# Optimization experiments

Measured on AMD Instinct MI355X. Metric: run time of the kernel, lower is better.

Reference implementation:

```python
import jax, jax.numpy as jnp
import numpy as np

B, T, C, H = 4, 2048, 1024, 16


def setup_inputs() -> dict:
    key = jax.random.key(0)
    k0, k1, k2 = jax.random.split(key, 3)
    s = C ** -0.5
    return {
        "x": jax.random.normal(k0, (B, T, C), jnp.float32),
        "Wqkv": jax.random.normal(k1, (C, 3 * C), jnp.float32) * s,
        "bqkv": jnp.zeros((3 * C,), jnp.float32),
        "Wo": jax.random.normal(k2, (C, C), jnp.float32) * s,
        "bo": jnp.zeros((C,), jnp.float32),
        "decoder": 1,
    }


def reference(x, Wqkv, bqkv, Wo, bo, decoder):
    Bx, Tx, Cx = x.shape
    d = Cx // H  # head dim
    qkv = x @ Wqkv + bqkv  # [B,T,3C]
    q, k, v = jnp.split(qkv, 3, axis=-1)
    q = q.reshape(Bx, Tx, H, d).transpose(0, 2, 1, 3)  # [B,H,T,d]
    k = k.reshape(Bx, Tx, H, d).transpose(0, 2, 1, 3)
    v = v.reshape(Bx, Tx, H, d).transpose(0, 2, 1, 3)
    # Source: qk / embd_dim**(-0.5)  ==  qk * sqrt(embd_dim)  (faithful quirk)
    scale = jnp.asarray(Cx ** 0.5, x.dtype)
    qk = jnp.einsum("bhqd,bhkd->bhqk", q, k) * scale  # [B,H,T,T]
    if decoder:  # decoder is a Python int constant
        tril = jnp.tril(jnp.ones((Tx, Tx), bool))
        qk = jnp.where(tril, qk, -jnp.inf)
    attn = jax.nn.softmax(qk, axis=-1)
    out = jnp.einsum("bhqk,bhkd->bhqd", attn, v)  # [B,H,T,d]
    out = out.transpose(0, 2, 1, 3).reshape(Bx, Tx, Cx)
    return out @ Wo + bo
```

## Files before the change

### kernel.cpp

```cpp
#include <hip/hip_runtime.h>
#include <cstdint>
#include <cstddef>

#define T_SEQ 2048
#define CEMB  1024
#define NHEAD 16
#define DHEAD 64

#define QSCALE 46.1662413084468f

typedef __attribute__((ext_vector_type(8))) short bf16x8;
typedef __attribute__((ext_vector_type(4))) float f32x4;

static __device__ __forceinline__ unsigned short f2bf(float x) {
    unsigned u = __builtin_bit_cast(unsigned, x);
    unsigned r = (u + 0x7FFFu + ((u >> 16) & 1u)) >> 16;
    return (unsigned short)r;
}
static __device__ __forceinline__ float bf2f(unsigned short b) {
    unsigned u = ((unsigned)b) << 16;
    return __builtin_bit_cast(float, u);
}

static __device__ __forceinline__ void gload16(const short* gsrc, short* ldsbase) {
    __builtin_amdgcn_global_load_lds(
        (const __attribute__((address_space(1))) void*)gsrc,
        (__attribute__((address_space(3))) void*)ldsbase, 16, 0, 0);
}

template<int SPLIT, bool A_F32, int OUT_MODE>
__global__ __launch_bounds__(256) void gemm_mfma_kernel(
    const float* __restrict__ Af, const short* __restrict__ Ah,
    const short* __restrict__ Bh, const short* __restrict__ Bl,
    const float* __restrict__ bias,
    void* __restrict__ Cout, void* __restrict__ Cout2, int K, int ldc)
{
    __shared__ __align__(16) short smem[(SPLIT == 3) ? 16384 : 8192];

    const int tid = threadIdx.x;
    const int w = tid >> 6, l = tid & 63;
    const int lr = l & 15, lg = l >> 4;
    const int wr = w >> 1, wc = w & 1;
    const int row0 = blockIdx.y * 128;
    const int col0 = blockIdx.x * 128;

    f32x4 acc[4][4];
    #pragma unroll
    for (int mt = 0; mt < 4; ++mt)
        #pragma unroll
        for (int nt = 0; nt < 4; ++nt)
            acc[mt][nt] = (f32x4){0.f, 0.f, 0.f, 0.f};

    const int sB0 = w * 128 + l, sB1 = sB0 + 64;
    const short* gB0 = Bh + (size_t)(col0 + (sB0 & 127)) * K + (sB0 >> 7) * 8;
    const short* gB1 = Bh + (size_t)(col0 + (sB1 & 127)) * K + (sB1 >> 7) * 8;
    short* dB0 = &smem[4096 + (w * 128) * 8];
    short* dB1 = &smem[4096 + (w * 128 + 64) * 8];
    const short* gBl0 = nullptr; const short* gBl1 = nullptr;
    if constexpr (SPLIT == 3) {
        gBl0 = Bl + (size_t)(col0 + (sB0 & 127)) * K + (sB0 >> 7) * 8;
        gBl1 = Bl + (size_t)(col0 + (sB1 & 127)) * K + (sB1 >> 7) * 8;
    }
    const short* gA0 = nullptr; const short* gA1 = nullptr;
    if constexpr (!A_F32) {
        gA0 = Ah + (size_t)(row0 + (sB0 & 127)) * K + (sB0 >> 7) * 8;
        gA1 = Ah + (size_t)(row0 + (sB1 & 127)) * K + (sB1 >> 7) * 8;
    }
    short* dA0 = &smem[(w * 128) * 8];
    short* dA1 = &smem[(w * 128 + 64) * 8];

    const int arow = tid >> 1, ahalf = tid & 1;
    const float* gAf = A_F32 ? (Af + (size_t)(row0 + arow) * K + ahalf * 16) : nullptr;

    for (int kt = 0; kt < K; kt += 32) {
        __syncthreads();
        if constexpr (!A_F32) {
            gload16(gA0 + kt, dA0);
            gload16(gA1 + kt, dA1);
        }
        gload16(gB0 + kt, dB0);
        gload16(gB1 + kt, dB1);
        if constexpr (SPLIT == 3) {
            gload16(gBl0 + kt, &smem[12288 + (w * 128) * 8]);
            gload16(gBl1 + kt, &smem[12288 + (w * 128 + 64) * 8]);
        }
        if constexpr (A_F32) {
            const float* src = gAf + kt;
            float4 f0 = *(const float4*)(src);
            float4 f1 = *(const float4*)(src + 4);
            float4 f2 = *(const float4*)(src + 8);
            float4 f3 = *(const float4*)(src + 12);
            float xs[16] = {f0.x, f0.y, f0.z, f0.w, f1.x, f1.y, f1.z, f1.w,
                            f2.x, f2.y, f2.z, f2.w, f3.x, f3.y, f3.z, f3.w};
            #pragma unroll
            for (int q = 0; q < 2; ++q) {
                bf16x8 h8, l8;
                #pragma unroll
                for (int e = 0; e < 8; ++e) {
                    float x = xs[q * 8 + e];
                    if constexpr (SPLIT == 3) {
                        unsigned u = __builtin_bit_cast(unsigned, x);
                        h8[e] = (short)(unsigned short)(u >> 16);
                        float hf = __builtin_bit_cast(float, u & 0xFFFF0000u);
                        l8[e] = (short)f2bf(x - hf);
                    } else {
                        h8[e] = (short)f2bf(x);
                    }
                }
                int slot = (ahalf * 2 + q) * 128 + arow;
                *(bf16x8*)&smem[slot * 8] = h8;
                if constexpr (SPLIT == 3) *(bf16x8*)&smem[8192 + slot * 8] = l8;
            }
        }
        __syncthreads();

        const int aoff = (lg * 128 + wr * 64 + lr) * 8;
        const int boff = 4096 + (lg * 128 + wc * 64 + lr) * 8;
        bf16x8 ahf[4], alf[4];
        #pragma unroll
        for (int mt = 0; mt < 4; ++mt) {
            ahf[mt] = *(const bf16x8*)&smem[aoff + mt * 128];
            if constexpr (SPLIT == 3)
                alf[mt] = *(const bf16x8*)&smem[8192 + aoff + mt * 128];
        }
        #pragma unroll
        for (int nt = 0; nt < 4; ++nt) {
            bf16x8 bhf = *(const bf16x8*)&smem[boff + nt * 128];
            if constexpr (SPLIT == 3) {
                bf16x8 blf = *(const bf16x8*)&smem[8192 + boff + nt * 128];
                #pragma unroll
                for (int mt = 0; mt < 4; ++mt) {
                    acc[mt][nt] = __builtin_amdgcn_mfma_f32_16x16x32_bf16(ahf[mt], bhf, acc[mt][nt], 0, 0, 0);
                    acc[mt][nt] = __builtin_amdgcn_mfma_f32_16x16x32_bf16(alf[mt], bhf, acc[mt][nt], 0, 0, 0);
                    acc[mt][nt] = __builtin_amdgcn_mfma_f32_16x16x32_bf16(ahf[mt], blf, acc[mt][nt], 0, 0, 0);
                }
            } else {
                #pragma unroll
                for (int mt = 0; mt < 4; ++mt)
                    acc[mt][nt] = __builtin_amdgcn_mfma_f32_16x16x32_bf16(ahf[mt], bhf, acc[mt][nt], 0, 0, 0);
            }
        }
    }

    #pragma unroll
    for (int mt = 0; mt < 4; ++mt) {
        #pragma unroll
        for (int r = 0; r < 4; ++r) {
            int m = row0 + wr * 64 + mt * 16 + lg * 4 + r;
            #pragma unroll
            for (int nt = 0; nt < 4; ++nt) {
                int n = col0 + wc * 64 + nt * 16 + lr;
                float v = acc[mt][nt][r] + bias[n];
                if constexpr (OUT_MODE == 0) {
                    ((float*)Cout)[(size_t)m * ldc + n] = v;
                } else if constexpr (OUT_MODE == 1) {
                    ((short*)Cout)[(size_t)m * ldc + n] = (short)f2bf(v);
                } else {
                    if (n < 1024) v *= QSCALE;
                    unsigned u = __builtin_bit_cast(unsigned, v);
                    ((short*)Cout)[(size_t)m * ldc + n] = (short)(unsigned short)(u >> 16);
                    float hf = __builtin_bit_cast(float, u & 0xFFFF0000u);
                    ((short*)Cout2)[(size_t)m * ldc + n] = (short)f2bf(v - hf);
                }
            }
        }
    }
}

__global__ __launch_bounds__(256) void transpose_split_kernel(
    const float* __restrict__ src, int nsrc,
    short* __restrict__ hi, short* __restrict__ lo)
{
    __shared__ float tile[64][68];
    const int tid = threadIdx.x;
    const int n0 = blockIdx.x * 64, k0 = blockIdx.y * 64;
    {
        int kr = tid >> 2, cg = tid & 3;
        const float* s = src + (size_t)(k0 + kr) * nsrc + n0 + cg * 16;
        #pragma unroll
        for (int q = 0; q < 4; ++q) {
            float4 f = *(const float4*)(s + q * 4);
            tile[kr][cg * 16 + q * 4 + 0] = f.x;
            tile[kr][cg * 16 + q * 4 + 1] = f.y;
            tile[kr][cg * 16 + q * 4 + 2] = f.z;
            tile[kr][cg * 16 + q * 4 + 3] = f.w;
        }
    }
    __syncthreads();
    {
        int nr = tid >> 2, kg = tid & 3;
        int n = n0 + nr;
        bf16x8 h0, h1, lo0, lo1;
        #pragma unroll
        for (int e = 0; e < 8; ++e) {
            float a = tile[kg * 16 + e][nr];
            float b = tile[kg * 16 + 8 + e][nr];
            unsigned short ha = f2bf(a), hb = f2bf(b);
            h0[e] = (short)ha; h1[e] = (short)hb;
            lo0[e] = (short)f2bf(a - bf2f(ha));
            lo1[e] = (short)f2bf(b - bf2f(hb));
        }
        short* dh = hi + (size_t)n * 1024 + k0 + kg * 16;
        *(bf16x8*)dh = h0;
        *(bf16x8*)(dh + 8) = h1;
        if (lo) {
            short* dl = lo + (size_t)n * 1024 + k0 + kg * 16;
            *(bf16x8*)dl = lo0;
            *(bf16x8*)(dl + 8) = lo1;
        }
    }
}

__global__ __launch_bounds__(256) void repack_vt_kernel(
    const short* __restrict__ v, short* __restrict__ vt)
{
    __shared__ short tile[64][80];
    const int tid = threadIdx.x;
    const int tt = blockIdx.x, h = blockIdx.y, b = blockIdx.z;
    const int t0 = tt * 64;
    {
        int tr = tid >> 2, cgrp = tid & 3;
        const short* src = v + (size_t)(b * T_SEQ + t0 + tr) * CEMB + h * DHEAD + cgrp * 16;
        *(bf16x8*)&tile[tr][cgrp * 16]     = *(const bf16x8*)src;
        *(bf16x8*)&tile[tr][cgrp * 16 + 8] = *(const bf16x8*)(src + 8);
    }
    __syncthreads();
    {
        int d = tid >> 2, tc = tid & 3;
        short s[16];
        #pragma unroll
        for (int e = 0; e < 16; ++e) s[e] = tile[tc * 16 + e][d];
        short* dst = vt + ((size_t)((b * NHEAD + h) * DHEAD + d)) * T_SEQ + t0 + tc * 16;
        bf16x8 v0, v1;
        #pragma unroll
        for (int e = 0; e < 8; ++e) { v0[e] = s[e]; v1[e] = s[8 + e]; }
        *(bf16x8*)dst       = v0;
        *(bf16x8*)(dst + 8) = v1;
    }
}

__global__ __launch_bounds__(256) void attn_mfma_kernel(
    const short* __restrict__ qkhi, const short* __restrict__ qklo,
    const short* __restrict__ vt, short* __restrict__ ctxb)
{
    __shared__ __align__(16) short smem[16384];

    const int tid = threadIdx.x;
    const int w = tid >> 6, l = tid & 63;
    const int lr = l & 15, lg = l >> 4;

    const int bid = blockIdx.x;
    const int p  = bid >> 6;
    const int bh = bid & 63;
    const int h = bh & 15, b = bh >> 4;
    const size_t bT = (size_t)b * T_SEQ;

    const int g0 = w * 128 + l, g1 = g0 + 64;
    const int rg0 = g0 >> 3, rg1 = g1 >> 3;
    const int sc0 = (g0 & 7) ^ (rg0 & 7), sc1 = (g1 & 7) ^ (rg1 & 7);
    short* const dst0 = &smem[(w * 128) * 8];
    short* const dst1 = &smem[(w * 128 + 64) * 8];

    const size_t koff0 = (bT + rg0) * 2048 + 1024 + h * DHEAD + sc0 * 8;
    const size_t koff1 = (bT + rg1) * 2048 + 1024 + h * DHEAD + sc1 * 8;
    const short* const pKh0 = qkhi + koff0;
    const short* const pKh1 = qkhi + koff1;
    const short* const pKl0 = qklo + koff0;
    const short* const pKl1 = qklo + koff1;
    const short* const pV0 = vt + ((size_t)((b * NHEAD + h) * DHEAD) + rg0) * T_SEQ + sc0 * 8;
    const short* const pV1 = vt + ((size_t)((b * NHEAD + h) * DHEAD) + rg1) * T_SEQ + sc1 * 8;

    const int psBase = 12288 + w * 1024;
    const int pwChunk = (lg >> 1);
    const int pwIntra = (lg & 1) * 4;

    for (int half = 0; half < 2; ++half) {
        const int xi = half ? (31 - p) : p;
        const int q0 = xi * 64;
        const int qw = q0 + w * 16;

        bf16x8 qhi[2], qlo[2];
        #pragma unroll
        for (int kk = 0; kk < 2; ++kk) {
            size_t off = (bT + qw + lr) * 2048 + h * DHEAD + kk * 32 + lg * 8;
            qhi[kk] = *(const bf16x8*)(qkhi + off);
            qlo[kk] = *(const bf16x8*)(qklo + off);
        }

        f32x4 O[4];
        #pragma unroll
        for (int dt = 0; dt < 4; ++dt)
            O[dt] = (f32x4){0.f, 0.f, 0.f, 0.f};
        float mrow = -3.0e38f;
        float lrow = 0.f;

        const int nsteps = xi + 1;
        for (int t = 0; t < nsteps; ++t) {
            const int j0 = t * 64;
            __syncthreads();
            gload16(pKh0 + (size_t)j0 * 2048, dst0);
            gload16(pKh1 + (size_t)j0 * 2048, dst1);
            gload16(pKl0 + (size_t)j0 * 2048, dst0 + 4096);
            gload16(pKl1 + (size_t)j0 * 2048, dst1 + 4096);
            gload16(pV0 + j0, dst0 + 8192);
            gload16(pV1 + j0, dst1 + 8192);
            __syncthreads();

            f32x4 St[4];
            #pragma unroll
            for (int ct = 0; ct < 4; ++ct) {
                f32x4 s = (f32x4){0.f, 0.f, 0.f, 0.f};
                #pragma unroll
                for (int kk = 0; kk < 2; ++kk) {
                    int j  = ct * 16 + lr;
                    int ck = kk * 4 + lg;
                    int idx = j * 64 + ((ck ^ (j & 7)) << 3);
                    bf16x8 kh8 = *(bf16x8*)&smem[idx];
                    bf16x8 kl8 = *(bf16x8*)&smem[4096 + idx];
                    s = __builtin_amdgcn_mfma_f32_16x16x32_bf16(kh8, qhi[kk], s, 0, 0, 0);
                    s = __builtin_amdgcn_mfma_f32_16x16x32_bf16(kh8, qlo[kk], s, 0, 0, 0);
                    s = __builtin_amdgcn_mfma_f32_16x16x32_bf16(kl8, qhi[kk], s, 0, 0, 0);
                }
                if (j0 + ct * 16 + 15 > qw) {
                    #pragma unroll
                    for (int r = 0; r < 4; ++r) {
                        int jabs = j0 + ct * 16 + lg * 4 + r;
                        int qabs = qw + lr;
                        s[r] = (jabs <= qabs) ? s[r] : -3.0e38f;
                    }
                }
                St[ct] = s;
            }

            float tm = fmaxf(fmaxf(fmaxf(St[0][0], St[0][1]), fmaxf(St[0][2], St[0][3])),
                             fmaxf(fmaxf(St[1][0], St[1][1]), fmaxf(St[1][2], St[1][3])));
            tm = fmaxf(tm, fmaxf(fmaxf(fmaxf(St[2][0], St[2][1]), fmaxf(St[2][2], St[2][3])),
                                 fmaxf(fmaxf(St[3][0], St[3][1]), fmaxf(St[3][2], St[3][3]))));
            tm = fmaxf(tm, __shfl_xor(tm, 16));
            tm = fmaxf(tm, __shfl_xor(tm, 32));

            if (__any(tm > mrow)) {
                float mnew  = fmaxf(mrow, tm);
                float alpha = __builtin_amdgcn_exp2f(mrow - mnew);
                mrow = mnew;
                lrow *= alpha;
                #pragma unroll
                for (int r = 0; r < 4; ++r) {
                    float aO = __shfl(alpha, lg * 4 + r);
                    #pragma unroll
                    for (int dt = 0; dt < 4; ++dt)
                        O[dt][r] *= aO;
                }
            }

            #pragma unroll
            for (int ct = 0; ct < 4; ++ct) {
                float p0 = __builtin_amdgcn_exp2f(St[ct][0] - mrow);
                float p1 = __builtin_amdgcn_exp2f(St[ct][1] - mrow);
                float p2 = __builtin_amdgcn_exp2f(St[ct][2] - mrow);
                float p3 = __builtin_amdgcn_exp2f(St[ct][3] - mrow);
                lrow += (p0 + p1) + (p2 + p3);
                unsigned u0 = (__builtin_bit_cast(unsigned, p0) >> 16) |
                              (__builtin_bit_cast(unsigned, p1) & 0xFFFF0000u);
                unsigned u1 = (__builtin_bit_cast(unsigned, p2) >> 16) |
                              (__builtin_bit_cast(unsigned, p3) & 0xFFFF0000u);
                int chunk = ct * 2 + pwChunk;
                int sidx = psBase + lr * 64 + ((chunk ^ (lr & 7)) << 3) + pwIntra;
                uint2 uu; uu.x = u0; uu.y = u1;
                *(uint2*)&smem[sidx] = uu;
            }

            __builtin_amdgcn_wave_barrier();

            bf16x8 pa[2];
            #pragma unroll
            for (int jk = 0; jk < 2; ++jk) {
                int ck = jk * 4 + lg;
                pa[jk] = *(bf16x8*)&smem[psBase + lr * 64 + ((ck ^ (lr & 7)) << 3)];
            }
            #pragma unroll
            for (int dt = 0; dt < 4; ++dt) {
                #pragma unroll
                for (int jk = 0; jk < 2; ++jk) {
                    int d  = dt * 16 + lr;
                    int ck = jk * 4 + lg;
                    bf16x8 vb = *(bf16x8*)&smem[8192 + d * 64 + ((ck ^ (d & 7)) << 3)];
                    O[dt] = __builtin_amdgcn_mfma_f32_16x16x32_bf16(pa[jk], vb, O[dt], 0, 0, 0);
                }
            }
        }

        float lsum = lrow + __shfl_xor(lrow, 16);
        lsum += __shfl_xor(lsum, 32);
        #pragma unroll
        for (int r = 0; r < 4; ++r) {
            float lO = __shfl(lsum, lg * 4 + r);
            float inv = 1.0f / lO;
            int row = qw + lg * 4 + r;
            #pragma unroll
            for (int dt = 0; dt < 4; ++dt) {
                int col = h * DHEAD + dt * 16 + lr;
                ctxb[(size_t)(b * T_SEQ + row) * CEMB + col] = (short)f2bf(O[dt][r] * inv);
            }
        }
    }
}

extern "C" void kernel_launch(void* const* d_in, const int* in_sizes, int n_in,
                              void* d_out, int out_size, void* d_ws, size_t ws_size,
                              hipStream_t stream)
{
    const float* x    = (const float*)d_in[0];
    const float* Wqkv = (const float*)d_in[1];
    const float* bqkv = (const float*)d_in[2];
    const float* Wo   = (const float*)d_in[3];
    const float* bo   = (const float*)d_in[4];
    float* out = (float*)d_out;

    char* ws = (char*)d_ws;
    short* qkhi = (short*)ws;
    short* vbuf = (short*)ws;
    short* qklo = (short*)(ws + (size_t)(32u << 20));
    short* Vt   = (short*)(ws + (size_t)(64u << 20));
    short* ctxb = (short*)(ws + (size_t)(80u << 20));
    short* WhiT = (short*)(ws + (size_t)(96u << 20));
    short* WloT = (short*)(ws + (size_t)(102u << 20));
    short* WoT  = (short*)(ws + (size_t)(108u << 20));

    transpose_split_kernel<<<dim3(48, 16), 256, 0, stream>>>(Wqkv, 3 * CEMB, WhiT, WloT);
    transpose_split_kernel<<<dim3(16, 16), 256, 0, stream>>>(Wo, CEMB, WoT, nullptr);

    gemm_mfma_kernel<1, true, 1><<<dim3(8, 64), 256, 0, stream>>>(
        x, nullptr, WhiT + (size_t)2048 * 1024, nullptr, bqkv + 2048, vbuf, nullptr, CEMB, CEMB);

    repack_vt_kernel<<<dim3(32, 16, 4), 256, 0, stream>>>(vbuf, Vt);

    gemm_mfma_kernel<3, true, 2><<<dim3(16, 64), 256, 0, stream>>>(
        x, nullptr, WhiT, WloT, bqkv, qkhi, qklo, CEMB, 2048);

    attn_mfma_kernel<<<dim3(1024), 256, 0, stream>>>(qkhi, qklo, Vt, ctxb);

    gemm_mfma_kernel<1, false, 0><<<dim3(8, 64), 256, 0, stream>>>(
        nullptr, ctxb, WoT, nullptr, bo, out, nullptr, CEMB, CEMB);
}
```

Measured before the change: 348.9 us.

## Pre-split x to bf16 hi/lo and double-buffer K/V loads in attention

A new kernel splits x into bf16 hi/lo arrays once, so the QKV GEMMs load A through async global-to-LDS copies instead of converting fp32 in every tile. The attention kernel now prefetches the next K tile and double-buffers V in a larger LDS area, overlapping loads with MFMA work, and raises wave priority around the MFMA sections. The V projection now uses the truncated x hi part rather than round-to-nearest bf16, which slightly changes rounding. The extra split pass and larger LDS footprint may reduce occupancy.

```diff
diff --git a/kernel.cpp b/kernel.cpp
--- a/kernel.cpp
+++ b/kernel.cpp
@@ -28,9 +28,28 @@
         (__attribute__((address_space(3))) void*)ldsbase, 16, 0, 0);
 }
 
-template<int SPLIT, bool A_F32, int OUT_MODE>
+__global__ __launch_bounds__(256) void split_x_kernel(
+    const float* __restrict__ x, short* __restrict__ hi, short* __restrict__ lo)
+{
+    size_t base = ((size_t)blockIdx.x * 256 + threadIdx.x) * 8;
+    float4 f0 = *(const float4*)(x + base);
+    float4 f1 = *(const float4*)(x + base + 4);
+    float xs[8] = {f0.x, f0.y, f0.z, f0.w, f1.x, f1.y, f1.z, f1.w};
+    bf16x8 h8, l8;
+    #pragma unroll
+    for (int e = 0; e < 8; ++e) {
+        unsigned u = __builtin_bit_cast(unsigned, xs[e]);
+        h8[e] = (short)(unsigned short)(u >> 16);
+        float hf = __builtin_bit_cast(float, u & 0xFFFF0000u);
+        l8[e] = (short)f2bf(xs[e] - hf);
+    }
+    *(bf16x8*)(hi + base) = h8;
+    *(bf16x8*)(lo + base) = l8;
+}
+
+template<int SPLIT, int OUT_MODE>
 __global__ __launch_bounds__(256) void gemm_mfma_kernel(
-    const float* __restrict__ Af, const short* __restrict__ Ah,
+    const short* __restrict__ Ah, const short* __restrict__ Al,
     const short* __restrict__ Bh, const short* __restrict__ Bl,
     const float* __restrict__ bias,
     void* __restrict__ Cout, void* __restrict__ Cout2, int K, int ldc)
@@ -51,83 +70,52 @@
         for (int nt = 0; nt < 4; ++nt)
             acc[mt][nt] = (f32x4){0.f, 0.f, 0.f, 0.f};
 
-    const int sB0 = w * 128 + l, sB1 = sB0 + 64;
-    const short* gB0 = Bh + (size_t)(col0 + (sB0 & 127)) * K + (sB0 >> 7) * 8;
-    const short* gB1 = Bh + (size_t)(col0 + (sB1 & 127)) * K + (sB1 >> 7) * 8;
-    short* dB0 = &smem[4096 + (w * 128) * 8];
-    short* dB1 = &smem[4096 + (w * 128 + 64) * 8];
+    const int s0 = w * 128 + l, s1 = s0 + 64;
+    const size_t aoff0 = (size_t)(row0 + (s0 & 127)) * K + (s0 >> 7) * 8;
+    const size_t aoff1 = (size_t)(row0 + (s1 & 127)) * K + (s1 >> 7) * 8;
+    const size_t boff0 = (size_t)(col0 + (s0 & 127)) * K + (s0 >> 7) * 8;
+    const size_t boff1 = (size_t)(col0 + (s1 & 127)) * K + (s1 >> 7) * 8;
+    const short* gA0 = Ah + aoff0;  const short* gA1 = Ah + aoff1;
+    const short* gB0 = Bh + boff0;  const short* gB1 = Bh + boff1;
+    const short* gAl0 = nullptr; const short* gAl1 = nullptr;
     const short* gBl0 = nullptr; const short* gBl1 = nullptr;
     if constexpr (SPLIT == 3) {
-        gBl0 = Bl + (size_t)(col0 + (sB0 & 127)) * K + (sB0 >> 7) * 8;
-        gBl1 = Bl + (size_t)(col0 + (sB1 & 127)) * K + (sB1 >> 7) * 8;
-    }
-    const short* gA0 = nullptr; const short* gA1 = nullptr;
-    if constexpr (!A_F32) {
-        gA0 = Ah + (size_t)(row0 + (sB0 & 127)) * K + (sB0 >> 7) * 8;
-        gA1 = Ah + (size_t)(row0 + (sB1 & 127)) * K + (sB1 >> 7) * 8;
-    }
-    short* dA0 = &smem[(w * 128) * 8];
-    short* dA1 = &smem[(w * 128 + 64) * 8];
-
-    const int arow = tid >> 1, ahalf = tid & 1;
-    const float* gAf = A_F32 ? (Af + (size_t)(row0 + arow) * K + ahalf * 16) : nullptr;
+        gAl0 = Al + aoff0;  gAl1 = Al + aoff1;
+        gBl0 = Bl + boff0;  gBl1 = Bl + boff1;
+    }
+    short* const dA0 = &smem[(w * 128) * 8];
+    short* const dA1 = &smem[(w * 128 + 64) * 8];
+    short* const dB0 = &smem[4096 + (w * 128) * 8];
+    short* const dB1 = &smem[4096 + (w * 128 + 64) * 8];
 
     for (int kt = 0; kt < K; kt += 32) {
         __syncthreads();
-        if constexpr (!A_F32) {
-            gload16(gA0 + kt, dA0);
-            gload16(gA1 + kt, dA1);
-        }
+        gload16(gA0 + kt, dA0);
+        gload16(gA1 + kt, dA1);
         gload16(gB0 + kt, dB0);
         gload16(gB1 + kt, dB1);
         if constexpr (SPLIT == 3) {
-            gload16(gBl0 + kt, &smem[12288 + (w * 128) * 8]);
-            gload16(gBl1 + kt, &smem[12288 + (w * 128 + 64) * 8]);
-        }
-        if constexpr (A_F32) {
-            const float* src = gAf + kt;
-            float4 f0 = *(const float4*)(src);
-            float4 f1 = *(const float4*)(src + 4);
-            float4 f2 = *(const float4*)(src + 8);
-            float4 f3 = *(const float4*)(src + 12);
-            float xs[16] = {f0.x, f0.y, f0.z, f0.w, f1.x, f1.y, f1.z, f1.w,
-                            f2.x, f2.y, f2.z, f2.w, f3.x, f3.y, f3.z, f3.w};
-            #pragma unroll
-            for (int q = 0; q < 2; ++q) {
-                bf16x8 h8, l8;
-                #pragma unroll
-                for (int e = 0; e < 8; ++e) {
-                    float x = xs[q * 8 + e];
-                    if constexpr (SPLIT == 3) {
-                        unsigned u = __builtin_bit_cast(unsigned, x);
-                        h8[e] = (short)(unsigned short)(u >> 16);
-                        float hf = __builtin_bit_cast(float, u & 0xFFFF0000u);
-                        l8[e] = (short)f2bf(x - hf);
-                    } else {
-                        h8[e] = (short)f2bf(x);
-                    }
-                }
-                int slot = (ahalf * 2 + q) * 128 + arow;
-                *(bf16x8*)&smem[slot * 8] = h8;
-                if constexpr (SPLIT == 3) *(bf16x8*)&smem[8192 + slot * 8] = l8;
-            }
+            gload16(gAl0 + kt, dA0 + 8192);
+            gload16(gAl1 + kt, dA1 + 8192);
+            gload16(gBl0 + kt, dB0 + 8192);
+            gload16(gBl1 + kt, dB1 + 8192);
         }
         __syncthreads();
 
-        const int aoff = (lg * 128 + wr * 64 + lr) * 8;
-        const int boff = 4096 + (lg * 128 + wc * 64 + lr) * 8;
+        const int ao = (lg * 128 + wr * 64 + lr) * 8;
+        const int bo = 4096 + (lg * 128 + wc * 64 + lr) * 8;
         bf16x8 ahf[4], alf[4];
         #pragma unroll
         for (int mt = 0; mt < 4; ++mt) {
-            ahf[mt] = *(const bf16x8*)&smem[aoff + mt * 128];
+            ahf[mt] = *(const bf16x8*)&smem[ao + mt * 128];
             if constexpr (SPLIT == 3)
-                alf[mt] = *(const bf16x8*)&smem[8192 + aoff + mt * 128];
+                alf[mt] = *(const bf16x8*)&smem[8192 + ao + mt * 128];
         }
         #pragma unroll
         for (int nt = 0; nt < 4; ++nt) {
-            bf16x8 bhf = *(const bf16x8*)&smem[boff + nt * 128];
+            bf16x8 bhf = *(const bf16x8*)&smem[bo + nt * 128];
             if constexpr (SPLIT == 3) {
-                bf16x8 blf = *(const bf16x8*)&smem[8192 + boff + nt * 128];
+                bf16x8 blf = *(const bf16x8*)&smem[8192 + bo + nt * 128];
                 #pragma unroll
                 for (int mt = 0; mt < 4; ++mt) {
                     acc[mt][nt] = __builtin_amdgcn_mfma_f32_16x16x32_bf16(ahf[mt], bhf, acc[mt][nt], 0, 0, 0);
@@ -243,7 +231,7 @@
     const short* __restrict__ qkhi, const short* __restrict__ qklo,
     const short* __restrict__ vt, short* __restrict__ ctxb)
 {
-    __shared__ __align__(16) short smem[16384];
+    __shared__ __align__(16) short smem[20480];
 
     const int tid = threadIdx.x;
     const int w = tid >> 6, l = tid & 63;
@@ -258,8 +246,8 @@
     const int g0 = w * 128 + l, g1 = g0 + 64;
     const int rg0 = g0 >> 3, rg1 = g1 >> 3;
     const int sc0 = (g0 & 7) ^ (rg0 & 7), sc1 = (g1 & 7) ^ (rg1 & 7);
-    short* const dst0 = &smem[(w * 128) * 8];
-    short* const dst1 = &smem[(w * 128 + 64) * 8];
+    short* const dK0 = &smem[(w * 128) * 8];
+    short* const dK1 = &smem[(w * 128 + 64) * 8];
 
     const size_t koff0 = (bT + rg0) * 2048 + 1024 + h * DHEAD + sc0 * 8;
     const size_t koff1 = (bT + rg1) * 2048 + 1024 + h * DHEAD + sc1 * 8;
@@ -270,14 +258,16 @@
     const short* const pV0 = vt + ((size_t)((b * NHEAD + h) * DHEAD) + rg0) * T_SEQ + sc0 * 8;
     const short* const pV1 = vt + ((size_t)((b * NHEAD + h) * DHEAD) + rg1) * T_SEQ + sc1 * 8;
 
-    const int psBase = 12288 + w * 1024;
+    const int psBase = 16384 + w * 1024;
     const int pwChunk = (lg >> 1);
     const int pwIntra = (lg & 1) * 4;
 
     for (int half = 0; half < 2; ++half) {
         const int xi = half ? (31 - p) : p;
-        const int q0 = xi * 64;
-        const int qw = q0 + w * 16;
+        const int qw = xi * 64 + w * 16;
+        const int nsteps = xi + 1;
+
+        __syncthreads();
 
         bf16x8 qhi[2], qlo[2];
         #pragma unroll
@@ -286,6 +276,19 @@
             qhi[kk] = *(const bf16x8*)(qkhi + off);
             qlo[kk] = *(const bf16x8*)(qklo + off);
         }
+        __builtin_amdgcn_sched_barrier(0);
+
+        gload16(pKh0, dK0);
+        gload16(pKh1, dK1);
+        gload16(pKl0, dK0 + 4096);
+        gload16(pKl1, dK1 + 4096);
+        gload16(pV0, dK0 + 8192);
+        gload16(pV1, dK1 + 8192);
+        {
+            int j1 = (nsteps > 1) ? 64 : 0;
+            gload16(pV0 + j1, dK0 + 12288);
+            gload16(pV1 + j1, dK1 + 12288);
+        }
 
         f32x4 O[4];
         #pragma unroll
@@ -294,19 +297,15 @@
         float mrow = -3.0e38f;
         float lrow = 0.f;
 
-        const int nsteps = xi + 1;
         for (int t = 0; t < nsteps; ++t) {
             const int j0 = t * 64;
-            __syncthreads();
-            gload16(pKh0 + (size_t)j0 * 2048, dst0);
-            gload16(pKh1 + (size_t)j0 * 2048, dst1);
-            gload16(pKl0 + (size_t)j0 * 2048, dst0 + 4096);
-            gload16(pKl1 + (size_t)j0 * 2048, dst1 + 4096);
-            gload16(pV0 + j0, dst0 + 8192);
-            gload16(pV1 + j0, dst1 + 8192);
-            __syncthreads();
+            asm volatile("s_waitcnt vmcnt(2)" ::: "memory");
+            __builtin_amdgcn_s_barrier();
+            __builtin_amdgcn_sched_barrier(0);
+            const int vbase = 8192 + (t & 1) * 4096;
 
             f32x4 St[4];
+            __builtin_amdgcn_s_setprio(1);
             #pragma unroll
             for (int ct = 0; ct < 4; ++ct) {
                 f32x4 s = (f32x4){0.f, 0.f, 0.f, 0.f};
@@ -321,15 +320,18 @@
                     s = __builtin_amdgcn_mfma_f32_16x16x32_bf16(kh8, qlo[kk], s, 0, 0, 0);
                     s = __builtin_amdgcn_mfma_f32_16x16x32_bf16(kl8, qhi[kk], s, 0, 0, 0);
                 }
+                St[ct] = s;
+            }
+            __builtin_amdgcn_s_setprio(0);
+            #pragma unroll
+            for (int ct = 0; ct < 4; ++ct) {
                 if (j0 + ct * 16 + 15 > qw) {
                     #pragma unroll
                     for (int r = 0; r < 4; ++r) {
                         int jabs = j0 + ct * 16 + lg * 4 + r;
-                        int qabs = qw + lr;
-                        s[r] = (jabs <= qabs) ? s[r] : -3.0e38f;
+                        St[ct][r] = (jabs <= qw + lr) ? St[ct][r] : -3.0e38f;
                     }
                 }
-                St[ct] = s;
             }
 
             float tm = fmaxf(fmaxf(fmaxf(St[0][0], St[0][1]), fmaxf(St[0][2], St[0][3])),
@@ -378,15 +380,33 @@
                 int ck = jk * 4 + lg;
                 pa[jk] = *(bf16x8*)&smem[psBase + lr * 64 + ((ck ^ (lr & 7)) << 3)];
             }
+            __builtin_amdgcn_s_setprio(1);
             #pragma unroll
             for (int dt = 0; dt < 4; ++dt) {
                 #pragma unroll
                 for (int jk = 0; jk < 2; ++jk) {
                     int d  = dt * 16 + lr;
                     int ck = jk * 4 + lg;
-                    bf16x8 vb = *(bf16x8*)&smem[8192 + d * 64 + ((ck ^ (d & 7)) << 3)];
+                    bf16x8 vb = *(bf16x8*)&smem[vbase + d * 64 + ((ck ^ (d & 7)) << 3)];
                     O[dt] = __builtin_amdgcn_mfma_f32_16x16x32_bf16(pa[jk], vb, O[dt], 0, 0, 0);
                 }
+            }
+            __builtin_amdgcn_s_setprio(0);
+
+            __builtin_amdgcn_sched_barrier(0);
+            __builtin_amdgcn_s_barrier();
+            __builtin_amdgcn_sched_barrier(0);
+
+            if (t + 1 < nsteps) {
+                size_t ko = (size_t)(t + 1) * 131072;
+                gload16(pKh0 + ko, dK0);
+                gload16(pKh1 + ko, dK1);
+                gload16(pKl0 + ko, dK0 + 4096);
+                gload16(pKl1 + ko, dK1 + 4096);
+                int jv = (t + 2 < nsteps) ? (t + 2) : (nsteps - 1);
+                short* const dV = &smem[8192 + (t & 1) * 4096];
+                gload16(pV0 + jv * 64, dV + (w * 128) * 8);
+                gload16(pV1 + jv * 64, dV + (w * 128 + 64) * 8);
             }
         }
 
@@ -419,10 +439,12 @@
 
     char* ws = (char*)d_ws;
     short* qkhi = (short*)ws;
-    short* vbuf = (short*)ws;
     short* qklo = (short*)(ws + (size_t)(32u << 20));
-    short* Vt   = (short*)(ws + (size_t)(64u << 20));
-    short* ctxb = (short*)(ws + (size_t)(80u << 20));
+    short* xlo  = (short*)(ws + (size_t)(64u << 20));
+    short* vbuf = xlo;
+    short* ctxb = xlo;
+    short* xhi  = (short*)(ws + (size_t)(80u << 20));
+    short* Vt   = xhi;
     short* WhiT = (short*)(ws + (size_t)(96u << 20));
     short* WloT = (short*)(ws + (size_t)(102u << 20));
     short* WoT  = (short*)(ws + (size_t)(108u << 20));
@@ -430,16 +452,19 @@
     transpose_split_kernel<<<dim3(48, 16), 256, 0, stream>>>(Wqkv, 3 * CEMB, WhiT, WloT);
     transpose_split_kernel<<<dim3(16, 16), 256, 0, stream>>>(Wo, CEMB, WoT, nullptr);
 
-    gemm_mfma_kernel<1, true, 1><<<dim3(8, 64), 256, 0, stream>>>(
-        x, nullptr, WhiT + (size_t)2048 * 1024, nullptr, bqkv + 2048, vbuf, nullptr, CEMB, CEMB);
+    split_x_kernel<<<dim3(4096), 256, 0, stream>>>(x, xhi, xlo);
+
+    gemm_mfma_kernel<3, 2><<<dim3(16, 64), 256, 0, stream>>>(
+        xhi, xlo, WhiT, WloT, bqkv, qkhi, qklo, CEMB, 2048);
+
+    gemm_mfma_kernel<1, 1><<<dim3(8, 64), 256, 0, stream>>>(
+        xhi, nullptr, WhiT + (size_t)2048 * 1024, nullptr, bqkv + 2048,
+        vbuf, nullptr, CEMB, CEMB);
 
     repack_vt_kernel<<<dim3(32, 16, 4), 256, 0, stream>>>(vbuf, Vt);
 
-    gemm_mfma_kernel<3, true, 2><<<dim3(16, 64), 256, 0, stream>>>(
-        x, nullptr, WhiT, WloT, bqkv, qkhi, qklo, CEMB, 2048);
-
     attn_mfma_kernel<<<dim3(1024), 256, 0, stream>>>(qkhi, qklo, Vt, ctxb);
 
-    gemm_mfma_kernel<1, false, 0><<<dim3(8, 64), 256, 0, stream>>>(
-        nullptr, ctxb, WoT, nullptr, bo, out, nullptr, CEMB, CEMB);
-}
+    gemm_mfma_kernel<1, 0><<<dim3(8, 64), 256, 0, stream>>>(
+        ctxb, nullptr, WoT, nullptr, bo, out, nullptr, CEMB, CEMB);
+}
```

Result: slower. 359.4 us (+3.0%).
